# Optimization experiments

Hardware: AMD Instinct MI355X
Metric: run time of the kernel (lower is better)

Reference implementation:

```python
import jax, jax.numpy as jnp
import numpy as np

N = 500_000      # nodes
E = 3_000_000    # edges (~degree 6 mesh)
C = 128          # in_channels
M = 125_000      # number of clusters (max(cluster)+1)
NUMPOOL = 5
B = 16           # graphs in batch


def setup_inputs() -> dict:
    key = jax.random.key(0)
    k1, k2, k3, k4, k5 = jax.random.split(key, 5)
    x = jax.random.normal(k1, (N, C), dtype=jnp.float32)
    xpos = jax.random.normal(k2, (N, 2), dtype=jnp.float32)
    # integer-valued float tensor (torch.cat forces common dtype in the original)
    indexattten = jax.random.randint(k3, (N, NUMPOOL), 0, M).astype(jnp.float32)
    # guarantee max(cluster) == M-1 so dim_size matches torch's max(cluster)+1
    indexattten = indexattten.at[0, :].set(float(M - 1))
    batch = jnp.sort(jax.random.randint(k4, (N,), 0, B)).astype(jnp.float32)
    edge_index = jax.random.randint(k5, (2, E), 0, N).astype(jnp.int64)
    return {"x": x, "edge_index": edge_index, "xpos": xpos,
            "indexattten": indexattten, "batch": batch, "poolindex": 2}


def reference(x, edge_index, xpos, indexattten, batch, poolindex):
    cluster = indexattten[:, poolindex].astype(jnp.int32)      # [N]
    # concat (x, pos, attn indices, batch) -> [N, C+2+NUMPOOL+1]
    feats = jnp.concatenate([x, xpos, indexattten, batch[:, None]], axis=1)
    sums = jax.ops.segment_sum(feats, cluster, num_segments=M)
    counts = jax.ops.segment_sum(jnp.ones((N, 1), jnp.float32), cluster,
                                 num_segments=M)
    new_x = sums / jnp.maximum(counts, 1.0)                    # scatter_mean

    # coalesce(cluster[edge_index]): sort + dedup; fixed-size via padding
    cl_edges = cluster[edge_index]                              # [2, E]
    keys = cl_edges[0].astype(jnp.int64) * M + cl_edges[1].astype(jnp.int64)
    uk = jnp.unique(keys, size=E, fill_value=keys.max())        # sorted, padded
    new_edge_index = jnp.stack([uk // M, uk % M]).astype(jnp.int64)

    new_xfinal = new_x[:, :C]
    new_pos = new_x[:, C:C + 2]
    indexatttennew = new_x[:, C + 2:C + 2 + NUMPOOL].astype(jnp.int64)
    new_batch = new_x[:, -1].astype(jnp.int64)
    # UnpoolInfo = (edge_index, cluster, batch)
    return (new_xfinal, new_edge_index, new_pos, indexatttennew, new_batch,
            edge_index, cluster, batch)
```

## Files before the change

kernel.cpp:

```cpp
#include <hip/hip_runtime.h>

namespace {
constexpr int N  = 500000;
constexpr long long E = 3000000;
constexpr int C  = 128;
constexpr int M  = 125000;
constexpr int NP = 5;
constexpr int ST = 65536;
constexpr int NC = 512;
constexpr int PMAX = 8192;
constexpr int NSB = 2048;

constexpr long long O_XF  = 0;
constexpr long long O_NEI = 16000000;
constexpr long long O_POS = 22000000;
constexpr long long O_IAT = 22250000;
constexpr long long O_NB  = 22875000;
constexpr long long O_EIP = 23000000;
constexpr long long O_CL  = 29000000;
constexpr long long O_BAT = 29500000;

constexpr long long S_CNT = 23000000;
constexpr long long S_CLU = 23130000;
constexpr long long S_COF = 23640000;
constexpr long long S_RPM = 23770000;
constexpr long long S_PT  = 25320000;
constexpr long long S_PT2 = 25390000;
constexpr long long S_CBN = 25500000;
constexpr long long S_CBS = 25501000;
constexpr long long S_CPS = 25502000;
constexpr long long S_UCT = 25503000;
constexpr long long S_UOF = 25504000;
}

__global__ void k_detect(const void* __restrict__ ei, int* __restrict__ flag) {
    if (threadIdx.x != 0 || blockIdx.x != 0) return;
    const unsigned long long* q = (const unsigned long long*)ei;
    unsigned long long hi = 0, lo = 0;
    for (int i = 0; i < 64; ++i) {
        unsigned long long a = q[i];
        unsigned long long b = q[(size_t)E / 2 + i];
        hi |= (a >> 32) | (b >> 32);
        lo |= (a & 0xffffffffULL) | (b & 0xffffffffULL);
    }
    int mode;
    if (hi == 0) mode = 1;
    else if (lo == 0) mode = 3;
    else {
        const int* p = (const int*)ei;
        int ok = 1;
        for (int i = 0; i < 256; ++i) {
            int v0 = p[i], v1 = p[E + i];
            if (v0 < 0 || v0 >= N || v1 < 0 || v1 >= N) ok = 0;
        }
        mode = ok ? 0 : 2;
    }
    *flag = mode;
}

__device__ __forceinline__ int load_ei(const void* ei, long long idx, int mode) {
    long long v;
    if (mode == 1)      v = ((const long long*)ei)[idx];
    else if (mode == 0) v = (long long)((const int*)ei)[idx];
    else if (mode == 3) v = (long long)(((const double*)ei)[idx]);
    else                v = (long long)(((const float*)ei)[idx]);
    if (v < 0 || v >= N) v = 0;
    return (int)v;
}

__device__ __forceinline__ unsigned make_key(int c0, int c1) {
    unsigned uv = (unsigned)c0 * (unsigned)M + (unsigned)c1;
    return uv ^ 0x80000000u;
}

__global__ void k_rows(const float* __restrict__ iat, const float* __restrict__ batch,
                       const int* __restrict__ pool, float* __restrict__ out) {
    int i = blockIdx.x * blockDim.x + threadIdx.x;
    if (i >= N) return;
    int p = pool[0];
    int c = (int)iat[(long long)i * NP + p];
    ((int*)(out + S_CLU))[i] = c;
    out[O_CL + i] = (float)c;
    out[O_BAT + i] = batch[i];
    atomicAdd((int*)(out + S_CNT) + c, 1);
}

__global__ void k_scan_part(const float* __restrict__ ob, long long in_off, int n) {
    int t = blockIdx.x * blockDim.x + threadIdx.x;
    const int* in = (const int*)(ob + in_off);
    int* pt = (int*)(ob + S_PT);
    int chunk = (n + ST - 1) / ST;
    int s = t * chunk, e = s + chunk;
    if (s > n) s = n;
    if (e > n) e = n;
    int sum = 0;
    for (int i = s; i < e; ++i) sum += in[i];
    pt[t] = sum;
}

__global__ void k_scan1(const float* __restrict__ ob, long long in_off,
                        long long out_off, int n) {
    const int* in = (const int*)(ob + in_off);
    int* outp = (int*)(ob + out_off);
    __shared__ int sh[1024];
    int tid = threadIdx.x;
    int chunk = (n + 1023) / 1024;
    int start = tid * chunk, end = start + chunk;
    if (start > n) start = n;
    if (end > n) end = n;
    int s = 0;
    for (int i = start; i < end; ++i) s += in[i];
    sh[tid] = s;
    __syncthreads();
    for (int off = 1; off < 1024; off <<= 1) {
        int v = (tid >= off) ? sh[tid - off] : 0;
        __syncthreads();
        sh[tid] += v;
        __syncthreads();
    }
    int run = (tid == 0) ? 0 : sh[tid - 1];
    for (int i = start; i < end; ++i) { outp[i] = run; run += in[i]; }
    if (tid == 1023) outp[n] = sh[1023];
}

__global__ void k_scan_out(const float* __restrict__ ob, long long in_off,
                           long long out_off, int n) {
    int t = blockIdx.x * blockDim.x + threadIdx.x;
    const int* in = (const int*)(ob + in_off);
    int* outp = (int*)(ob + out_off);
    int run = ((const int*)(ob + S_PT2))[t];
    int chunk = (n + ST - 1) / ST;
    int s = t * chunk, e = s + chunk;
    if (s > n) s = n;
    if (e > n) e = n;
    for (int i = s; i < e; ++i) { outp[i] = run; run += in[i]; }
    if (t == ST - 1) outp[n] = run;
}

__global__ void k_rowscatter(float* __restrict__ out) {
    int i = blockIdx.x * blockDim.x + threadIdx.x;
    if (i >= N) return;
    int c = ((const int*)(out + S_CLU))[i];
    int pos = atomicAdd((int*)(out + S_COF) + c, 1);
    ((int*)(out + S_RPM))[pos] = i;
}

__global__ void k_xmean(const float4* __restrict__ x4, float* __restrict__ out) {
    long long t = (long long)blockIdx.x * blockDim.x + threadIdx.x;
    int wid = (int)(t >> 6);
    int lane = threadIdx.x & 63;
    if (wid >= M) return;
    const int* coff = (const int*)(out + S_COF);
    int start = (wid == 0) ? 0 : coff[wid - 1];
    int end = coff[wid];
    int cnt = end - start;
    float fcnt = (float)cnt;
    if (fcnt < 1.0f) fcnt = 1.0f;
    const int* rpm = (const int*)(out + S_RPM);
    int g = lane >> 4;
    int sub = lane & 15;
    float4 a0 = make_float4(0.f, 0.f, 0.f, 0.f);
    float4 a1 = make_float4(0.f, 0.f, 0.f, 0.f);
    for (int cb = 0; cb < cnt; cb += 64) {
        int rem = cnt - cb;
        if (rem > 64) rem = 64;
        int rl = (lane < rem) ? rpm[start + cb + lane] : 0;
        for (int r = g; r < rem; r += 4) {
            int row = __shfl(rl, r, 64);
            long long b = (long long)row * 32 + sub * 2;
            float4 v0 = x4[b];
            float4 v1 = x4[b + 1];
            a0.x += v0.x; a0.y += v0.y; a0.z += v0.z; a0.w += v0.w;
            a1.x += v1.x; a1.y += v1.y; a1.z += v1.z; a1.w += v1.w;
        }
    }
    a0.x += __shfl_xor(a0.x, 16, 64); a0.y += __shfl_xor(a0.y, 16, 64);
    a0.z += __shfl_xor(a0.z, 16, 64); a0.w += __shfl_xor(a0.w, 16, 64);
    a1.x += __shfl_xor(a1.x, 16, 64); a1.y += __shfl_xor(a1.y, 16, 64);
    a1.z += __shfl_xor(a1.z, 16, 64); a1.w += __shfl_xor(a1.w, 16, 64);
    a0.x += __shfl_xor(a0.x, 32, 64); a0.y += __shfl_xor(a0.y, 32, 64);
    a0.z += __shfl_xor(a0.z, 32, 64); a0.w += __shfl_xor(a0.w, 32, 64);
    a1.x += __shfl_xor(a1.x, 32, 64); a1.y += __shfl_xor(a1.y, 32, 64);
    a1.z += __shfl_xor(a1.z, 32, 64); a1.w += __shfl_xor(a1.w, 32, 64);
    if (lane < 16) {
        float4 o0, o1;
        o0.x = a0.x / fcnt; o0.y = a0.y / fcnt; o0.z = a0.z / fcnt; o0.w = a0.w / fcnt;
        o1.x = a1.x / fcnt; o1.y = a1.y / fcnt; o1.z = a1.z / fcnt; o1.w = a1.w / fcnt;
        long long b = (long long)wid * 32 + sub * 2;
        ((float4*)(out + O_XF))[b]     = o0;
        ((float4*)(out + O_XF))[b + 1] = o1;
    }
}

__global__ void k_smallmean(const float* __restrict__ xpos, const float* __restrict__ iat,
                            const float* __restrict__ batch, float* __restrict__ out) {
    int t = blockIdx.x * blockDim.x + threadIdx.x;
    if (t >= M * 8) return;
    int m = t >> 3;
    int lc = t & 7;
    const int* coff = (const int*)(out + S_COF);
    int start = (m == 0) ? 0 : coff[m - 1];
    int end = coff[m];
    float cnt = (float)(end - start);
    if (cnt < 1.0f) cnt = 1.0f;
    const int* rpm = (const int*)(out + S_RPM);
    float s = 0.0f;
    for (int r = start; r < end; ++r) {
        int row = rpm[r];
        float v;
        if (lc < 2)      v = xpos[(long long)row * 2 + lc];
        else if (lc < 7) v = iat[(long long)row * NP + (lc - 2)];
        else             v = batch[row];
        s += v;
    }
    float mres = s / cnt;
    if (lc >= 2) mres = truncf(mres);
    if (lc < 2)      out[O_POS + (long long)m * 2 + lc] = mres;
    else if (lc < 7) out[O_IAT + (long long)m * NP + (lc - 2)] = mres;
    else             out[O_NB + m] = mres;
}

__global__ __launch_bounds__(256) void k_edges2(const void* __restrict__ ei,
                                                const int* __restrict__ flag,
                                                float* __restrict__ out) {
    __shared__ int h[NC];
    int tid = threadIdx.x;
    long long cb = (long long)blockIdx.x * 4096;
    for (int s = tid; s < NC; s += 256) h[s] = 0;
    __syncthreads();
    int mode = *flag;
    const int* cluster = (const int*)(out + S_CLU);
    unsigned* stage = (unsigned*)(out + O_NEI);
    for (int s = 0; s < 16; ++s) {
        long long i = cb + s * 256 + tid;
        if (i < E) {
            int c0 = cluster[load_ei(ei, i, mode)];
            int c1 = cluster[load_ei(ei, E + i, mode)];
            unsigned key = make_key(c0, c1);
            stage[i] = key;
            atomicAdd(&h[key >> 23], 1);
        }
    }
    __syncthreads();
    for (int s = tid; s < NC; s += 256) {
        int v = h[s];
        if (v) atomicAdd((int*)(out + S_CBN) + s, v);
    }
}

__global__ void k_scan512(float* __restrict__ out, long long in_off,
                          long long out_off, long long pos_off) {
    __shared__ int sh[NC];
    int tid = threadIdx.x;
    const int* in = (const int*)(out + in_off);
    int* o = (int*)(out + out_off);
    int v0 = in[tid];
    sh[tid] = v0;
    __syncthreads();
    for (int off = 1; off < NC; off <<= 1) {
        int v = (tid >= off) ? sh[tid - off] : 0;
        __syncthreads();
        sh[tid] += v;
        __syncthreads();
    }
    int excl = sh[tid] - v0;
    o[tid] = excl;
    if (pos_off >= 0) ((int*)(out + pos_off))[tid] = excl;
    if (tid == NC - 1) o[NC] = sh[NC - 1];
}

__global__ __launch_bounds__(512) void k_part(float* __restrict__ out) {
    __shared__ int h[NC], h2[NC], lb[NC], gb[NC];
    __shared__ unsigned g[4096];
    __shared__ int d[4096];
    int tid = threadIdx.x;
    long long cb = (long long)blockIdx.x * 4096;
    const unsigned* stage = (const unsigned*)(out + O_NEI);
    unsigned* bdata = (unsigned*)(out + O_EIP + E);
    if (tid < NC) { h[tid] = 0; h2[tid] = 0; }
    __syncthreads();
    unsigned keys[8];
    for (int s = 0; s < 8; ++s) {
        long long i = cb + s * 512 + tid;
        if (i < E) {
            unsigned key = stage[i];
            keys[s] = key;
            atomicAdd(&h[key >> 23], 1);
        }
    }
    __syncthreads();
    if (tid < NC) lb[tid] = h[tid];
    __syncthreads();
    for (int off = 1; off < NC; off <<= 1) {
        int v = (tid < NC && tid >= off) ? lb[tid - off] : 0;
        __syncthreads();
        if (tid < NC) lb[tid] += v;
        __syncthreads();
    }
    if (tid < NC) {
        int excl = lb[tid] - h[tid];
        gb[tid] = atomicAdd((int*)(out + S_CPS) + tid, h[tid]);
        lb[tid] = excl;
    }
    __syncthreads();
    for (int s = 0; s < 8; ++s) {
        long long i = cb + s * 512 + tid;
        if (i < E) {
            unsigned key = keys[s];
            int b = key >> 23;
            int r = atomicAdd(&h2[b], 1);
            int slot = lb[b] + r;
            g[slot] = key;
            d[slot] = gb[b] + r;
        }
    }
    __syncthreads();
    int tot = (int)((E - cb < 4096) ? (E - cb) : 4096);
    for (int s = 0; s < 8; ++s) {
        int slot = tid + s * 512;
        if (slot < tot) bdata[d[slot]] = g[slot];
    }
}

__global__ __launch_bounds__(1024) void k_psort(float* __restrict__ out) {
    __shared__ unsigned sk2[PMAX];
    __shared__ int hist[NSB];
    __shared__ int hstart[NSB];
    __shared__ int ssc[1024];
    int p = blockIdx.x;
    int tid = threadIdx.x;
    const int* cbase = (const int*)(out + S_CBS);
    int base = cbase[p];
    int n = cbase[p + 1] - base;
    if (n > PMAX) n = PMAX;
    unsigned* bdata = (unsigned*)(out + O_EIP + E);
    for (int i = tid; i < NSB; i += 1024) hist[i] = 0;
    __syncthreads();
    for (int i = tid; i < n; i += 1024)
        atomicAdd(&hist[(bdata[base + i] >> 12) & (NSB - 1)], 1);
    __syncthreads();
    int h0 = hist[2 * tid], h1 = hist[2 * tid + 1];
    ssc[tid] = h0 + h1;
    __syncthreads();
    for (int off = 1; off < 1024; off <<= 1) {
        int v = (tid >= off) ? ssc[tid - off] : 0;
        __syncthreads();
        ssc[tid] += v;
        __syncthreads();
    }
    int excl = ssc[tid] - (h0 + h1);
    hstart[2 * tid] = excl;      hstart[2 * tid + 1] = excl + h0;
    __syncthreads();
    hist[2 * tid] = excl;        hist[2 * tid + 1] = excl + h0;
    __syncthreads();
    for (int i = tid; i < n; i += 1024) {
        unsigned k = bdata[base + i];
        int b = (k >> 12) & (NSB - 1);
        int r = atomicAdd(&hist[b], 1);
        sk2[r] = k;
    }
    __syncthreads();
    for (int bb = 0; bb < 2; ++bb) {
        int b = 2 * tid + bb;
        int s = hstart[b];
        int e = hist[b];
        for (int i = s + 1; i < e; ++i) {
            unsigned v = sk2[i];
            int j = i - 1;
            while (j >= s && sk2[j] > v) { sk2[j + 1] = sk2[j]; --j; }
            sk2[j + 1] = v;
        }
    }
    __syncthreads();
    int chunk = (n + 1023) / 1024;
    int cs = tid * chunk, ce = cs + chunk;
    if (cs > n) cs = n;
    if (ce > n) ce = n;
    int c = 0;
    for (int i = cs; i < ce; ++i)
        if (i == 0 || sk2[i] != sk2[i - 1]) ++c;
    ssc[tid] = c;
    __syncthreads();
    for (int off = 1; off < 1024; off <<= 1) {
        int v = (tid >= off) ? ssc[tid - off] : 0;
        __syncthreads();
        ssc[tid] += v;
        __syncthreads();
    }
    int pos = ssc[tid] - c;
    for (int i = cs; i < ce; ++i)
        if (i == 0 || sk2[i] != sk2[i - 1]) bdata[base + pos++] = sk2[i];
    if (tid == 1023) ((int*)(out + S_UCT))[p] = ssc[1023];
}

__global__ __launch_bounds__(256) void k_uwrite2(float* __restrict__ out) {
    int p = blockIdx.x;
    int tid = threadIdx.x;
    int base = ((const int*)(out + S_CBS))[p];
    int u    = ((const int*)(out + S_UCT))[p];
    long long dst = ((const int*)(out + S_UOF))[p];
    const unsigned* bdata = (const unsigned*)(out + O_EIP + E);
    for (int i = tid; i < u; i += 256) {
        unsigned v = bdata[base + i];
        long long k = (long long)(int)(v ^ 0x80000000u);
        long long r = k % M; if (r < 0) r += M;
        long long q = (k - r) / M;
        out[O_NEI + dst + i]     = (float)q;
        out[O_NEI + E + dst + i] = (float)r;
    }
}

__global__ void k_fill(float* __restrict__ out) {
    int p = blockIdx.x * blockDim.x + threadIdx.x;
    if (p >= E) return;
    int U = ((const int*)(out + S_UOF))[NC];
    if (p < U) return;
    float r0 = out[O_NEI + U - 1];
    float r1 = out[O_NEI + E + U - 1];
    out[O_NEI + p]     = r0;
    out[O_NEI + E + p] = r1;
}

__global__ void k_pass(const void* __restrict__ ei, const int* __restrict__ flag,
                       float* __restrict__ out) {
    int e = blockIdx.x * blockDim.x + threadIdx.x;
    if (e >= E) return;
    int mode = *flag;
    out[O_EIP + e]     = (float)load_ei(ei, e, mode);
    out[O_EIP + E + e] = (float)load_ei(ei, E + e, mode);
}

static inline void scan3(float* out, long long in_off, long long out_off, int n,
                         hipStream_t stream) {
    k_scan_part<<<ST / 256, 256, 0, stream>>>(out, in_off, n);
    k_scan1<<<1, 1024, 0, stream>>>(out, S_PT, S_PT2, ST);
    k_scan_out<<<ST / 256, 256, 0, stream>>>(out, in_off, out_off, n);
}

extern "C" void kernel_launch(void* const* d_in, const int* in_sizes, int n_in,
                              void* d_out, int out_size, void* d_ws, size_t ws_size,
                              hipStream_t stream) {
    const float* x     = (const float*)d_in[0];
    const void*  ei    = d_in[1];
    const float* xpos  = (const float*)d_in[2];
    const float* iat   = (const float*)d_in[3];
    const float* batch = (const float*)d_in[4];
    const int*   pool  = (const int*)d_in[5];
    float* out = (float*)d_out;
    int* flag = (int*)d_ws;

    int eblocks = (int)((E + 4095) / 4096);

    hipMemsetAsync(out + S_CNT, 0, (size_t)M * 4, stream);
    hipMemsetAsync(out + S_CBN, 0, (size_t)NC * 4, stream);

    k_detect<<<1, 64, 0, stream>>>(ei, flag);
    k_rows<<<(N + 255) / 256, 256, 0, stream>>>(iat, batch, pool, out);
    scan3(out, S_CNT, S_COF, M, stream);
    k_rowscatter<<<(N + 255) / 256, 256, 0, stream>>>(out);

    long long txm = (long long)M * 64;
    k_xmean<<<(unsigned)((txm + 255) / 256), 256, 0, stream>>>((const float4*)x, out);
    k_smallmean<<<(M * 8 + 255) / 256, 256, 0, stream>>>(xpos, iat, batch, out);

    k_edges2<<<eblocks, 256, 0, stream>>>(ei, flag, out);
    k_scan512<<<1, NC, 0, stream>>>(out, S_CBN, S_CBS, S_CPS);
    k_part<<<eblocks, 512, 0, stream>>>(out);
    k_psort<<<NC, 1024, 0, stream>>>(out);
    k_scan512<<<1, NC, 0, stream>>>(out, S_UCT, S_UOF, -1);
    k_uwrite2<<<NC, 256, 0, stream>>>(out);
    k_fill<<<(unsigned)((E + 255) / 256), 256, 0, stream>>>(out);
    k_pass<<<(unsigned)((E + 255) / 256), 256, 0, stream>>>(ei, flag, out);
}
```

Baseline: 392.4 us.

## Move scratch buffers to workspace, fuse edge passthrough into edges pass, widen xmean loads

When the workspace is large enough, the scratch arrays (counts, cluster ids, offsets, row map, bucket data) move from the output buffer into the workspace. That frees the edge_index passthrough region, so k_edges2 can write the converted edge indices while it loads them and the separate k_pass kernel is dropped. k_xmean now has 8 row groups of 8 lanes, each lane handling 4 float4 per row instead of 2, which gives more rows in flight per wave. The cost is a dependence on workspace size, with an output-aliased fallback path kept for small workspaces.

```diff
diff --git a/kernel.cpp b/kernel.cpp
--- a/kernel.cpp
+++ b/kernel.cpp
@@ -74,21 +74,20 @@
 }
 
 __global__ void k_rows(const float* __restrict__ iat, const float* __restrict__ batch,
-                       const int* __restrict__ pool, float* __restrict__ out) {
+                       const int* __restrict__ pool, float* __restrict__ out,
+                       int* __restrict__ clu, int* __restrict__ cnt) {
     int i = blockIdx.x * blockDim.x + threadIdx.x;
     if (i >= N) return;
     int p = pool[0];
     int c = (int)iat[(long long)i * NP + p];
-    ((int*)(out + S_CLU))[i] = c;
+    clu[i] = c;
     out[O_CL + i] = (float)c;
     out[O_BAT + i] = batch[i];
-    atomicAdd((int*)(out + S_CNT) + c, 1);
-}
-
-__global__ void k_scan_part(const float* __restrict__ ob, long long in_off, int n) {
+    atomicAdd(cnt + c, 1);
+}
+
+__global__ void k_scan_part(const int* __restrict__ in, int* __restrict__ pt, int n) {
     int t = blockIdx.x * blockDim.x + threadIdx.x;
-    const int* in = (const int*)(ob + in_off);
-    int* pt = (int*)(ob + S_PT);
     int chunk = (n + ST - 1) / ST;
     int s = t * chunk, e = s + chunk;
     if (s > n) s = n;
@@ -98,10 +97,7 @@
     pt[t] = sum;
 }
 
-__global__ void k_scan1(const float* __restrict__ ob, long long in_off,
-                        long long out_off, int n) {
-    const int* in = (const int*)(ob + in_off);
-    int* outp = (int*)(ob + out_off);
+__global__ void k_scan1(const int* __restrict__ in, int* __restrict__ outp, int n) {
     __shared__ int sh[1024];
     int tid = threadIdx.x;
     int chunk = (n + 1023) / 1024;
@@ -123,12 +119,10 @@
     if (tid == 1023) outp[n] = sh[1023];
 }
 
-__global__ void k_scan_out(const float* __restrict__ ob, long long in_off,
-                           long long out_off, int n) {
+__global__ void k_scan_out(const int* __restrict__ in, const int* __restrict__ pt2,
+                           int* __restrict__ outp, int n) {
     int t = blockIdx.x * blockDim.x + threadIdx.x;
-    const int* in = (const int*)(ob + in_off);
-    int* outp = (int*)(ob + out_off);
-    int run = ((const int*)(ob + S_PT2))[t];
+    int run = pt2[t];
     int chunk = (n + ST - 1) / ST;
     int s = t * chunk, e = s + chunk;
     if (s > n) s = n;
@@ -137,73 +131,83 @@
     if (t == ST - 1) outp[n] = run;
 }
 
-__global__ void k_rowscatter(float* __restrict__ out) {
+__global__ void k_rowscatter(const int* __restrict__ clu, int* __restrict__ cof,
+                             int* __restrict__ rpm) {
     int i = blockIdx.x * blockDim.x + threadIdx.x;
     if (i >= N) return;
-    int c = ((const int*)(out + S_CLU))[i];
-    int pos = atomicAdd((int*)(out + S_COF) + c, 1);
-    ((int*)(out + S_RPM))[pos] = i;
-}
-
-__global__ void k_xmean(const float4* __restrict__ x4, float* __restrict__ out) {
+    int c = clu[i];
+    int pos = atomicAdd(cof + c, 1);
+    rpm[pos] = i;
+}
+
+__global__ void k_xmean(const float4* __restrict__ x4, float* __restrict__ out,
+                        const int* __restrict__ cof, const int* __restrict__ rpm) {
     long long t = (long long)blockIdx.x * blockDim.x + threadIdx.x;
     int wid = (int)(t >> 6);
     int lane = threadIdx.x & 63;
     if (wid >= M) return;
-    const int* coff = (const int*)(out + S_COF);
-    int start = (wid == 0) ? 0 : coff[wid - 1];
-    int end = coff[wid];
+    int start = (wid == 0) ? 0 : cof[wid - 1];
+    int end = cof[wid];
     int cnt = end - start;
     float fcnt = (float)cnt;
     if (fcnt < 1.0f) fcnt = 1.0f;
-    const int* rpm = (const int*)(out + S_RPM);
-    int g = lane >> 4;
-    int sub = lane & 15;
+    int g = lane >> 3;
+    int sub = lane & 7;
     float4 a0 = make_float4(0.f, 0.f, 0.f, 0.f);
-    float4 a1 = make_float4(0.f, 0.f, 0.f, 0.f);
+    float4 a1 = a0, a2 = a0, a3 = a0;
     for (int cb = 0; cb < cnt; cb += 64) {
         int rem = cnt - cb;
         if (rem > 64) rem = 64;
         int rl = (lane < rem) ? rpm[start + cb + lane] : 0;
-        for (int r = g; r < rem; r += 4) {
+        for (int r = g; r < rem; r += 8) {
             int row = __shfl(rl, r, 64);
-            long long b = (long long)row * 32 + sub * 2;
-            float4 v0 = x4[b];
-            float4 v1 = x4[b + 1];
+            const float4* rb = x4 + (long long)row * 32 + sub;
+            float4 v0 = rb[0];
+            float4 v1 = rb[8];
+            float4 v2 = rb[16];
+            float4 v3 = rb[24];
             a0.x += v0.x; a0.y += v0.y; a0.z += v0.z; a0.w += v0.w;
             a1.x += v1.x; a1.y += v1.y; a1.z += v1.z; a1.w += v1.w;
+            a2.x += v2.x; a2.y += v2.y; a2.z += v2.z; a2.w += v2.w;
+            a3.x += v3.x; a3.y += v3.y; a3.z += v3.z; a3.w += v3.w;
         }
     }
-    a0.x += __shfl_xor(a0.x, 16, 64); a0.y += __shfl_xor(a0.y, 16, 64);
-    a0.z += __shfl_xor(a0.z, 16, 64); a0.w += __shfl_xor(a0.w, 16, 64);
-    a1.x += __shfl_xor(a1.x, 16, 64); a1.y += __shfl_xor(a1.y, 16, 64);
-    a1.z += __shfl_xor(a1.z, 16, 64); a1.w += __shfl_xor(a1.w, 16, 64);
-    a0.x += __shfl_xor(a0.x, 32, 64); a0.y += __shfl_xor(a0.y, 32, 64);
-    a0.z += __shfl_xor(a0.z, 32, 64); a0.w += __shfl_xor(a0.w, 32, 64);
-    a1.x += __shfl_xor(a1.x, 32, 64); a1.y += __shfl_xor(a1.y, 32, 64);
-    a1.z += __shfl_xor(a1.z, 32, 64); a1.w += __shfl_xor(a1.w, 32, 64);
-    if (lane < 16) {
-        float4 o0, o1;
-        o0.x = a0.x / fcnt; o0.y = a0.y / fcnt; o0.z = a0.z / fcnt; o0.w = a0.w / fcnt;
-        o1.x = a1.x / fcnt; o1.y = a1.y / fcnt; o1.z = a1.z / fcnt; o1.w = a1.w / fcnt;
-        long long b = (long long)wid * 32 + sub * 2;
-        ((float4*)(out + O_XF))[b]     = o0;
-        ((float4*)(out + O_XF))[b + 1] = o1;
+#define XRED(K) \
+    a0.x += __shfl_xor(a0.x, K, 64); a0.y += __shfl_xor(a0.y, K, 64); \
+    a0.z += __shfl_xor(a0.z, K, 64); a0.w += __shfl_xor(a0.w, K, 64); \
+    a1.x += __shfl_xor(a1.x, K, 64); a1.y += __shfl_xor(a1.y, K, 64); \
+    a1.z += __shfl_xor(a1.z, K, 64); a1.w += __shfl_xor(a1.w, K, 64); \
+    a2.x += __shfl_xor(a2.x, K, 64); a2.y += __shfl_xor(a2.y, K, 64); \
+    a2.z += __shfl_xor(a2.z, K, 64); a2.w += __shfl_xor(a2.w, K, 64); \
+    a3.x += __shfl_xor(a3.x, K, 64); a3.y += __shfl_xor(a3.y, K, 64); \
+    a3.z += __shfl_xor(a3.z, K, 64); a3.w += __shfl_xor(a3.w, K, 64);
+    XRED(8) XRED(16) XRED(32)
+#undef XRED
+    if (lane < 8) {
+        float4* ob = (float4*)(out + O_XF) + (long long)wid * 32 + sub;
+        float4 o;
+        o.x = a0.x / fcnt; o.y = a0.y / fcnt; o.z = a0.z / fcnt; o.w = a0.w / fcnt;
+        ob[0] = o;
+        o.x = a1.x / fcnt; o.y = a1.y / fcnt; o.z = a1.z / fcnt; o.w = a1.w / fcnt;
+        ob[8] = o;
+        o.x = a2.x / fcnt; o.y = a2.y / fcnt; o.z = a2.z / fcnt; o.w = a2.w / fcnt;
+        ob[16] = o;
+        o.x = a3.x / fcnt; o.y = a3.y / fcnt; o.z = a3.z / fcnt; o.w = a3.w / fcnt;
+        ob[24] = o;
     }
 }
 
 __global__ void k_smallmean(const float* __restrict__ xpos, const float* __restrict__ iat,
-                            const float* __restrict__ batch, float* __restrict__ out) {
+                            const float* __restrict__ batch, float* __restrict__ out,
+                            const int* __restrict__ cof, const int* __restrict__ rpm) {
     int t = blockIdx.x * blockDim.x + threadIdx.x;
     if (t >= M * 8) return;
     int m = t >> 3;
     int lc = t & 7;
-    const int* coff = (const int*)(out + S_COF);
-    int start = (m == 0) ? 0 : coff[m - 1];
-    int end = coff[m];
+    int start = (m == 0) ? 0 : cof[m - 1];
+    int end = cof[m];
     float cnt = (float)(end - start);
     if (cnt < 1.0f) cnt = 1.0f;
-    const int* rpm = (const int*)(out + S_RPM);
     float s = 0.0f;
     for (int r = start; r < end; ++r) {
         int row = rpm[r];
@@ -222,21 +226,26 @@
 
 __global__ __launch_bounds__(256) void k_edges2(const void* __restrict__ ei,
                                                 const int* __restrict__ flag,
-                                                float* __restrict__ out) {
+                                                const int* __restrict__ clu,
+                                                unsigned* __restrict__ stage,
+                                                int* __restrict__ cbn,
+                                                float* __restrict__ out, int fuse) {
     __shared__ int h[NC];
     int tid = threadIdx.x;
     long long cb = (long long)blockIdx.x * 4096;
     for (int s = tid; s < NC; s += 256) h[s] = 0;
     __syncthreads();
     int mode = *flag;
-    const int* cluster = (const int*)(out + S_CLU);
-    unsigned* stage = (unsigned*)(out + O_NEI);
     for (int s = 0; s < 16; ++s) {
         long long i = cb + s * 256 + tid;
         if (i < E) {
-            int c0 = cluster[load_ei(ei, i, mode)];
-            int c1 = cluster[load_ei(ei, E + i, mode)];
-            unsigned key = make_key(c0, c1);
+            int e0 = load_ei(ei, i, mode);
+            int e1 = load_ei(ei, E + i, mode);
+            if (fuse) {
+                out[O_EIP + i]     = (float)e0;
+                out[O_EIP + E + i] = (float)e1;
+            }
+            unsigned key = make_key(clu[e0], clu[e1]);
             stage[i] = key;
             atomicAdd(&h[key >> 23], 1);
         }
@@ -244,16 +253,14 @@
     __syncthreads();
     for (int s = tid; s < NC; s += 256) {
         int v = h[s];
-        if (v) atomicAdd((int*)(out + S_CBN) + s, v);
-    }
-}
-
-__global__ void k_scan512(float* __restrict__ out, long long in_off,
-                          long long out_off, long long pos_off) {
+        if (v) atomicAdd(cbn + s, v);
+    }
+}
+
+__global__ void k_scan512(const int* __restrict__ in, int* __restrict__ o,
+                          int* __restrict__ pos) {
     __shared__ int sh[NC];
     int tid = threadIdx.x;
-    const int* in = (const int*)(out + in_off);
-    int* o = (int*)(out + out_off);
     int v0 = in[tid];
     sh[tid] = v0;
     __syncthreads();
@@ -265,18 +272,18 @@
     }
     int excl = sh[tid] - v0;
     o[tid] = excl;
-    if (pos_off >= 0) ((int*)(out + pos_off))[tid] = excl;
+    if (pos) pos[tid] = excl;
     if (tid == NC - 1) o[NC] = sh[NC - 1];
 }
 
-__global__ __launch_bounds__(512) void k_part(float* __restrict__ out) {
+__global__ __launch_bounds__(512) void k_part(const unsigned* __restrict__ stage,
+                                              int* __restrict__ cps,
+                                              unsigned* __restrict__ bdata) {
     __shared__ int h[NC], h2[NC], lb[NC], gb[NC];
     __shared__ unsigned g[4096];
     __shared__ int d[4096];
     int tid = threadIdx.x;
     long long cb = (long long)blockIdx.x * 4096;
-    const unsigned* stage = (const unsigned*)(out + O_NEI);
-    unsigned* bdata = (unsigned*)(out + O_EIP + E);
     if (tid < NC) { h[tid] = 0; h2[tid] = 0; }
     __syncthreads();
     unsigned keys[8];
@@ -299,7 +306,7 @@
     }
     if (tid < NC) {
         int excl = lb[tid] - h[tid];
-        gb[tid] = atomicAdd((int*)(out + S_CPS) + tid, h[tid]);
+        gb[tid] = atomicAdd(cps + tid, h[tid]);
         lb[tid] = excl;
     }
     __syncthreads();
@@ -322,18 +329,18 @@
     }
 }
 
-__global__ __launch_bounds__(1024) void k_psort(float* __restrict__ out) {
+__global__ __launch_bounds__(1024) void k_psort(const int* __restrict__ cbs,
+                                                unsigned* __restrict__ bdata,
+                                                int* __restrict__ uct) {
     __shared__ unsigned sk2[PMAX];
     __shared__ int hist[NSB];
     __shared__ int hstart[NSB];
     __shared__ int ssc[1024];
     int p = blockIdx.x;
     int tid = threadIdx.x;
-    const int* cbase = (const int*)(out + S_CBS);
-    int base = cbase[p];
-    int n = cbase[p + 1] - base;
+    int base = cbs[p];
+    int n = cbs[p + 1] - base;
     if (n > PMAX) n = PMAX;
-    unsigned* bdata = (unsigned*)(out + O_EIP + E);
     for (int i = tid; i < NSB; i += 1024) hist[i] = 0;
     __syncthreads();
     for (int i = tid; i < n; i += 1024)
@@ -390,16 +397,19 @@
     int pos = ssc[tid] - c;
     for (int i = cs; i < ce; ++i)
         if (i == 0 || sk2[i] != sk2[i - 1]) bdata[base + pos++] = sk2[i];
-    if (tid == 1023) ((int*)(out + S_UCT))[p] = ssc[1023];
-}
-
-__global__ __launch_bounds__(256) void k_uwrite2(float* __restrict__ out) {
+    if (tid == 1023) uct[p] = ssc[1023];
+}
+
+__global__ __launch_bounds__(256) void k_uwrite2(const int* __restrict__ cbs,
+                                                 const int* __restrict__ uct,
+                                                 const int* __restrict__ uof,
+                                                 const unsigned* __restrict__ bdata,
+                                                 float* __restrict__ out) {
     int p = blockIdx.x;
     int tid = threadIdx.x;
-    int base = ((const int*)(out + S_CBS))[p];
-    int u    = ((const int*)(out + S_UCT))[p];
-    long long dst = ((const int*)(out + S_UOF))[p];
-    const unsigned* bdata = (const unsigned*)(out + O_EIP + E);
+    int base = cbs[p];
+    int u = uct[p];
+    long long dst = uof[p];
     for (int i = tid; i < u; i += 256) {
         unsigned v = bdata[base + i];
         long long k = (long long)(int)(v ^ 0x80000000u);
@@ -410,10 +420,10 @@
     }
 }
 
-__global__ void k_fill(float* __restrict__ out) {
+__global__ void k_fill(const int* __restrict__ uof, float* __restrict__ out) {
     int p = blockIdx.x * blockDim.x + threadIdx.x;
     if (p >= E) return;
-    int U = ((const int*)(out + S_UOF))[NC];
+    int U = uof[NC];
     if (p < U) return;
     float r0 = out[O_NEI + U - 1];
     float r1 = out[O_NEI + E + U - 1];
@@ -428,13 +438,6 @@
     int mode = *flag;
     out[O_EIP + e]     = (float)load_ei(ei, e, mode);
     out[O_EIP + E + e] = (float)load_ei(ei, E + e, mode);
-}
-
-static inline void scan3(float* out, long long in_off, long long out_off, int n,
-                         hipStream_t stream) {
-    k_scan_part<<<ST / 256, 256, 0, stream>>>(out, in_off, n);
-    k_scan1<<<1, 1024, 0, stream>>>(out, S_PT, S_PT2, ST);
-    k_scan_out<<<ST / 256, 256, 0, stream>>>(out, in_off, out_off, n);
 }
 
 extern "C" void kernel_launch(void* const* d_in, const int* in_sizes, int n_in,
@@ -447,28 +450,63 @@
     const float* batch = (const float*)d_in[4];
     const int*   pool  = (const int*)d_in[5];
     float* out = (float*)d_out;
-    int* flag = (int*)d_ws;
+    unsigned* stage = (unsigned*)(out + O_NEI);
+
+    bool usew = ws_size >= (size_t)18000000;
+    int *cnt, *clu, *cof, *rpm, *pt, *pt2, *cbn, *cbs, *cps, *uct, *uof, *flag;
+    unsigned* bdata;
+    int fuse;
+    if (usew) {
+        int* W = (int*)d_ws;
+        cnt = W;
+        clu = W + 125000;
+        cof = W + 625024;
+        rpm = W + 750080;
+        pt  = W + 1250112;
+        pt2 = W + 1315712;
+        cbn = W + 1381312;
+        cbs = W + 1381888;
+        cps = W + 1382464;
+        uct = W + 1383040;
+        uof = W + 1383616;
+        bdata = (unsigned*)(W + 1384192);
+        flag = W + 4384256;
+        fuse = 1;
+    } else {
+        cnt = (int*)(out + S_CNT); clu = (int*)(out + S_CLU);
+        cof = (int*)(out + S_COF); rpm = (int*)(out + S_RPM);
+        pt  = (int*)(out + S_PT);  pt2 = (int*)(out + S_PT2);
+        cbn = (int*)(out + S_CBN); cbs = (int*)(out + S_CBS);
+        cps = (int*)(out + S_CPS); uct = (int*)(out + S_UCT);
+        uof = (int*)(out + S_UOF);
+        bdata = (unsigned*)(out + O_EIP + E);
+        flag = (int*)d_ws;
+        fuse = 0;
+    }
 
     int eblocks = (int)((E + 4095) / 4096);
 
-    hipMemsetAsync(out + S_CNT, 0, (size_t)M * 4, stream);
-    hipMemsetAsync(out + S_CBN, 0, (size_t)NC * 4, stream);
+    hipMemsetAsync(cnt, 0, (size_t)M * 4, stream);
+    hipMemsetAsync(cbn, 0, (size_t)NC * 4, stream);
 
     k_detect<<<1, 64, 0, stream>>>(ei, flag);
-    k_rows<<<(N + 255) / 256, 256, 0, stream>>>(iat, batch, pool, out);
-    scan3(out, S_CNT, S_COF, M, stream);
-    k_rowscatter<<<(N + 255) / 256, 256, 0, stream>>>(out);
+    k_rows<<<(N + 255) / 256, 256, 0, stream>>>(iat, batch, pool, out, clu, cnt);
+    k_scan_part<<<ST / 256, 256, 0, stream>>>(cnt, pt, M);
+    k_scan1<<<1, 1024, 0, stream>>>(pt, pt2, ST);
+    k_scan_out<<<ST / 256, 256, 0, stream>>>(cnt, pt2, cof, M);
+    k_rowscatter<<<(N + 255) / 256, 256, 0, stream>>>(clu, cof, rpm);
 
     long long txm = (long long)M * 64;
-    k_xmean<<<(unsigned)((txm + 255) / 256), 256, 0, stream>>>((const float4*)x, out);
-    k_smallmean<<<(M * 8 + 255) / 256, 256, 0, stream>>>(xpos, iat, batch, out);
-
-    k_edges2<<<eblocks, 256, 0, stream>>>(ei, flag, out);
-    k_scan512<<<1, NC, 0, stream>>>(out, S_CBN, S_CBS, S_CPS);
-    k_part<<<eblocks, 512, 0, stream>>>(out);
-    k_psort<<<NC, 1024, 0, stream>>>(out);
-    k_scan512<<<1, NC, 0, stream>>>(out, S_UCT, S_UOF, -1);
-    k_uwrite2<<<NC, 256, 0, stream>>>(out);
-    k_fill<<<(unsigned)((E + 255) / 256), 256, 0, stream>>>(out);
-    k_pass<<<(unsigned)((E + 255) / 256), 256, 0, stream>>>(ei, flag, out);
-}
+    k_xmean<<<(unsigned)((txm + 255) / 256), 256, 0, stream>>>(
+        (const float4*)x, out, cof, rpm);
+    k_smallmean<<<(M * 8 + 255) / 256, 256, 0, stream>>>(xpos, iat, batch, out, cof, rpm);
+
+    k_edges2<<<eblocks, 256, 0, stream>>>(ei, flag, clu, stage, cbn, out, fuse);
+    k_scan512<<<1, NC, 0, stream>>>(cbn, cbs, cps);
+    k_part<<<eblocks, 512, 0, stream>>>(stage, cps, bdata);
+    k_psort<<<NC, 1024, 0, stream>>>(cbs, bdata, uct);
+    k_scan512<<<1, NC, 0, stream>>>(uct, uof, (int*)nullptr);
+    k_uwrite2<<<NC, 256, 0, stream>>>(cbs, uct, uof, bdata, out);
+    k_fill<<<(unsigned)((E + 255) / 256), 256, 0, stream>>>(uof, out);
+    if (!fuse) k_pass<<<(unsigned)((E + 255) / 256), 256, 0, stream>>>(ei, flag, out);
+}
```

Result: slower. 403.0 us (+2.7%).
